# Optimization experiments

Measured on AMD Instinct MI355X. Metric: run time of the kernel, lower is better.

Reference implementation:

```python
import jax, jax.numpy as jnp
import numpy as np

DROPOUT_P = 0.5
HALF_D_LOG_2PI = 8.0  # 0.5 * D * log(2*pi) constant from source, D=16


def _dropout(key, x, p):
    keep = 1.0 - p
    mask = jax.random.bernoulli(key, keep, x.shape).astype(x.dtype)
    return x * mask / keep


def _spmm(adj_vals, row, col, support, n):
    # out[i] = sum_{e: row[e]==i} adj_vals[e] * support[col[e]]
    return jax.ops.segment_sum(adj_vals[:, None] * support[col], row, num_segments=n)


def setup_inputs() -> dict:
    key = jax.random.key(0)
    ks = jax.random.split(key, 9)
    N, F_IN, D, C, E, K = 100000, 512, 16, 16, 3200000, 16
    return {
        "x": jax.random.normal(ks[0], (N, F_IN), dtype=jnp.float32),
        "W1": jax.random.normal(ks[1], (F_IN, D), dtype=jnp.float32) * 0.05,
        "W2": jax.random.normal(ks[2], (D, C), dtype=jnp.float32) * 0.2,
        "adj_vals": jax.random.uniform(ks[3], (E,), dtype=jnp.float32),
        "PI": jax.random.uniform(ks[4], (K,), dtype=jnp.float32, minval=0.01, maxval=1.0),
        "MUs": jax.random.normal(ks[5], (K, D), dtype=jnp.float32),
        "PREs": jax.random.uniform(ks[6], (K, D), dtype=jnp.float32, minval=0.1, maxval=1.0),
        "row": jnp.sort(jax.random.randint(ks[7], (E,), 0, N, dtype=jnp.int32)),
        "col": jax.random.randint(ks[8], (E,), 0, N, dtype=jnp.int32),
    }


def reference(x, W1, W2, adj_vals, PI, MUs, PREs, row, col):
    n = x.shape[0]
    dk1, dk2 = jax.random.split(jax.random.key(42))
    # layer 1: dropout -> linear (P1) -> spmm (P2)
    h = _spmm(adj_vals, row, col, _dropout(dk1, x, DROPOUT_P) @ W1, n)  # [N, D]
    # GMM log-likelihood: log N(h | MU_k, diag(1/PRE_k)) + log PI_k
    diff = h[:, None, :] - MUs[None, :, :]                      # [N, K, D]
    logcomp = (-0.5 * jnp.sum(diff * diff * PREs[None], axis=2)
               + jnp.log(PI)[None, :]
               + 0.5 * jnp.sum(jnp.log(PREs), axis=1)[None, :]
               - HALF_D_LOG_2PI * jnp.log(2.0 * jnp.pi))        # [N, K]
    probs = -jnp.mean(jnp.max(logcomp, axis=1))
    # layer 2: relu -> dropout -> linear -> spmm -> log_softmax
    x1 = jax.nn.relu(h)
    h2 = _spmm(adj_vals, row, col, _dropout(dk2, x1, DROPOUT_P) @ W2, n)  # [N, C]
    return jax.nn.log_softmax(h2, axis=1), probs
```

## Files before the change

### kernel.cpp

```cpp
#include <hip/hip_runtime.h>
#include <stdint.h>

typedef __attribute__((ext_vector_type(8))) short bf16x8;
typedef __attribute__((ext_vector_type(4))) float f32x4;
typedef __attribute__((ext_vector_type(4))) int i32x4;

__host__ __device__ __forceinline__ uint32_t rotl32(uint32_t x, int d){
  return (x << d) | (x >> (32 - d));
}

__host__ __device__ __forceinline__ void threefry2x32(uint32_t k0, uint32_t k1,
                                                      uint32_t x0, uint32_t x1,
                                                      uint32_t* o0, uint32_t* o1){
  uint32_t ks2 = k0 ^ k1 ^ 0x1BD11BDAu;
  x0 += k0; x1 += k1;
  x0 += x1; x1 = rotl32(x1,13); x1 ^= x0;
  x0 += x1; x1 = rotl32(x1,15); x1 ^= x0;
  x0 += x1; x1 = rotl32(x1,26); x1 ^= x0;
  x0 += x1; x1 = rotl32(x1, 6); x1 ^= x0;
  x0 += k1; x1 += ks2 + 1u;
  x0 += x1; x1 = rotl32(x1,17); x1 ^= x0;
  x0 += x1; x1 = rotl32(x1,29); x1 ^= x0;
  x0 += x1; x1 = rotl32(x1,16); x1 ^= x0;
  x0 += x1; x1 = rotl32(x1,24); x1 ^= x0;
  x0 += ks2; x1 += k0 + 2u;
  x0 += x1; x1 = rotl32(x1,13); x1 ^= x0;
  x0 += x1; x1 = rotl32(x1,15); x1 ^= x0;
  x0 += x1; x1 = rotl32(x1,26); x1 ^= x0;
  x0 += x1; x1 = rotl32(x1, 6); x1 ^= x0;
  x0 += k0; x1 += k1 + 3u;
  x0 += x1; x1 = rotl32(x1,17); x1 ^= x0;
  x0 += x1; x1 = rotl32(x1,29); x1 ^= x0;
  x0 += x1; x1 = rotl32(x1,16); x1 ^= x0;
  x0 += x1; x1 = rotl32(x1,24); x1 ^= x0;
  x0 += k1; x1 += ks2 + 4u;
  x0 += x1; x1 = rotl32(x1,13); x1 ^= x0;
  x0 += x1; x1 = rotl32(x1,15); x1 ^= x0;
  x0 += x1; x1 = rotl32(x1,26); x1 ^= x0;
  x0 += x1; x1 = rotl32(x1, 6); x1 ^= x0;
  x0 += ks2; x1 += k0 + 5u;
  *o0 = x0; *o1 = x1;
}

__device__ __forceinline__ uint32_t tf_dropbit(uint32_t k0, uint32_t k1, uint32_t j){
  uint32_t o0, o1;
  threefry2x32(k0, k1, 0u, j, &o0, &o1);
  return (o0 ^ o1) >> 31;
}

__device__ __forceinline__ uint32_t rotl1(uint32_t x, int d){
  return __builtin_amdgcn_alignbit(x, x, (uint32_t)(32 - d));
}

__device__ __forceinline__ ushort f2bf(float f){
  uint32_t u = __float_as_uint(f);
  u += 0x7FFFu + ((u >> 16) & 1u);
  return (ushort)(u >> 16);
}
__device__ __forceinline__ float bf2f(ushort b){
  return __uint_as_float(((uint32_t)b) << 16);
}

__device__ __forceinline__ uint2 drop4(uint32_t k0, uint32_t k1, uint32_t j,
                                       float f0, float f1, float f2, float f3){
  uint32_t ks2 = k0 ^ k1 ^ 0x1BD11BDAu;
  uint32_t xa0 = k0, xa1 = (j + 0u) + k1;
  uint32_t xb0 = k0, xb1 = (j + 1u) + k1;
  uint32_t xc0 = k0, xc1 = (j + 2u) + k1;
  uint32_t xd0 = k0, xd1 = (j + 3u) + k1;
#define RR(d)                                              \
  xa0 += xa1; xa1 = rotl1(xa1, d); xa1 ^= xa0;             \
  xb0 += xb1; xb1 = rotl1(xb1, d); xb1 ^= xb0;             \
  xc0 += xc1; xc1 = rotl1(xc1, d); xc1 ^= xc0;             \
  xd0 += xd1; xd1 = rotl1(xd1, d); xd1 ^= xd0;
#define INJ(ka, kb)                                        \
  { uint32_t A = (ka), B = (kb);                           \
    xa0 += A; xa1 += B; xb0 += A; xb1 += B;                \
    xc0 += A; xc1 += B; xd0 += A; xd1 += B; }
  RR(13) RR(15) RR(26) RR(6)  INJ(k1, ks2 + 1u)
  RR(17) RR(29) RR(16) RR(24) INJ(ks2, k0 + 2u)
  RR(13) RR(15) RR(26) RR(6)  INJ(k0, k1 + 3u)
  RR(17) RR(29) RR(16) RR(24) INJ(k1, ks2 + 4u)
  RR(13) RR(15) RR(26) RR(6)  INJ(ks2, k0 + 5u)
#undef RR
#undef INJ
  uint32_t ba = xa0 ^ xa1, bb = xb0 ^ xb1, bc = xc0 ^ xc1, bd = xd0 ^ xd1;
  uint32_t ua = __float_as_uint(f0) + 0x8000u;
  uint32_t ub = __float_as_uint(f1) + 0x8000u;
  uint32_t uc = __float_as_uint(f2) + 0x8000u;
  uint32_t ud = __float_as_uint(f3) + 0x8000u;
  uint32_t sa = (uint32_t)((int32_t)ba >> 31);
  uint32_t sb = (uint32_t)((int32_t)bb >> 31);
  uint32_t sc = (uint32_t)((int32_t)bc >> 31);
  uint32_t sd = (uint32_t)((int32_t)bd >> 31);
  uint32_t v01 = __builtin_amdgcn_perm(ub, ua, 0x07060302u);
  uint32_t v23 = __builtin_amdgcn_perm(ud, uc, 0x07060302u);
  uint32_t m01 = __builtin_amdgcn_perm(sb, sa, 0x07060302u);
  uint32_t m23 = __builtin_amdgcn_perm(sd, sc, 0x07060302u);
  return make_uint2(v01 & ~m01, v23 & ~m23);
}

__global__ void k_prep(const float* __restrict__ W1, ushort* __restrict__ w1p,
                       const float* __restrict__ PI, const float* __restrict__ PREs,
                       float* __restrict__ ckg){
  int t = threadIdx.x;
  for (int u = 0; u < 32; ++u){
    int idx = u * 256 + t;
    int k = idx >> 4, c = idx & 15;
    w1p[((k >> 3) * 16 + c) * 8 + (k & 7)] = f2bf(2.0f * W1[idx]);
  }
  if (t < 16){
    float s = logf(PI[t]);
    #pragma unroll
    for (int j = 0; j < 16; ++j) s += 0.5f * logf(PREs[t * 16 + j]);
    ckg[t] = s - 8.0f * logf(6.28318530717958647692f);
  }
}

__global__ __launch_bounds__(256, 4) void k_main(
    const float* __restrict__ x, const ushort* __restrict__ w1p,
    ushort* __restrict__ s1, const int* __restrict__ rowv, int* __restrict__ rp,
    uint32_t dk0, uint32_t dk1, int N, int E, int nbG, int nbR){
  __shared__ float part[4][16][17];
  int bid = blockIdx.x;
  if (bid % 5 != 0){
    int rb = bid - bid / 5 - 1;
    if (rb < nbR){
      int e = rb * 256 + threadIdx.x;
      if (e <= E){
        int r0 = (e > 0) ? rowv[e - 1] : -1;
        int r1 = (e < E) ? rowv[e] : N;
        for (int r = r0 + 1; r <= r1; ++r) rp[r] = e;
      }
    }
    return;
  }
  int gb = bid / 5;
  if (gb >= nbG) return;

  int t = threadIdx.x;
  int l = t & 63, w = t >> 6;
  int rA = l & 15, kg = l >> 4;
  int tb = w >> 1, p = w & 1;
  int r0 = gb * 32 + tb * 16;
  int rr = r0 + rA; if (rr > N - 1) rr = N - 1;
  const float4* xv = reinterpret_cast<const float4*>(
      x + (size_t)rr * 512 + (p * 256 + kg * 8));
  uint32_t jb = (uint32_t)rr * 512u + (uint32_t)(p * 256 + kg * 8);

  const bf16x8* bp = reinterpret_cast<const bf16x8*>(w1p);
  bf16x8 Bf[8];
  #pragma unroll
  for (int q = 0; q < 8; ++q) Bf[q] = bp[((p * 8 + q) * 4 + kg) * 16 + rA];

  float4 xa = xv[0], xb = xv[1];
  __builtin_amdgcn_sched_barrier(0);

  f32x4 acc = {0.f, 0.f, 0.f, 0.f};
  #pragma unroll
  for (int ks = 0; ks < 8; ++ks){
    float4 na, nb;
    if (ks < 7){ na = xv[(ks + 1) * 8]; nb = xv[(ks + 1) * 8 + 1]; }
    __builtin_amdgcn_sched_barrier(0);
    uint32_t j0 = jb + (uint32_t)(ks * 32);
    uint2 lo = drop4(dk0, dk1, j0,      xa.x, xa.y, xa.z, xa.w);
    uint2 hi = drop4(dk0, dk1, j0 + 4u, xb.x, xb.y, xb.z, xb.w);
    i32x4 ai = {(int)lo.x, (int)lo.y, (int)hi.x, (int)hi.y};
    bf16x8 a = __builtin_bit_cast(bf16x8, ai);
    acc = __builtin_amdgcn_mfma_f32_16x16x32_bf16(a, Bf[ks], acc, 0, 0, 0);
    if (ks < 7){ xa = na; xb = nb; }
  }

  #pragma unroll
  for (int i2 = 0; i2 < 4; ++i2) part[w][kg * 4 + i2][rA] = acc[i2];
  __syncthreads();
  #pragma unroll
  for (int q = 0; q < 2; ++q){
    int idx = q * 256 + t;
    int tt = idx >> 8, row = (idx >> 4) & 15, col = idx & 15;
    int n = gb * 32 + tt * 16 + row;
    float sum = part[tt * 2][row][col] + part[tt * 2 + 1][row][col];
    if (n < N) s1[(size_t)n * 16 + col] = f2bf(sum);
  }
}

__device__ __forceinline__ float edge_sum(const float* __restrict__ adj,
                                          const int* __restrict__ colv,
                                          const ushort* __restrict__ tbl_d,
                                          int e0, int e1){
  float hs = 0.f;
  int e = e0;
  int ea = (e0 + 3) & ~3; if (ea > e1) ea = e1;
  for (; e < ea; ++e) hs += adj[e] * bf2f(tbl_d[(size_t)colv[e] * 16]);
  float a0 = 0.f, a1 = 0.f, a2 = 0.f, a3 = 0.f;
  float b0 = 0.f, b1 = 0.f, b2 = 0.f, b3 = 0.f;
  for (; e + 8 <= e1; e += 8){
    float4 av = *reinterpret_cast<const float4*>(adj + e);
    int4   cv = *reinterpret_cast<const int4*>(colv + e);
    float4 aw = *reinterpret_cast<const float4*>(adj + e + 4);
    int4   cw = *reinterpret_cast<const int4*>(colv + e + 4);
    a0 += av.x * bf2f(tbl_d[(size_t)cv.x * 16]);
    a1 += av.y * bf2f(tbl_d[(size_t)cv.y * 16]);
    a2 += av.z * bf2f(tbl_d[(size_t)cv.z * 16]);
    a3 += av.w * bf2f(tbl_d[(size_t)cv.w * 16]);
    b0 += aw.x * bf2f(tbl_d[(size_t)cw.x * 16]);
    b1 += aw.y * bf2f(tbl_d[(size_t)cw.y * 16]);
    b2 += aw.z * bf2f(tbl_d[(size_t)cw.z * 16]);
    b3 += aw.w * bf2f(tbl_d[(size_t)cw.w * 16]);
  }
  if (e + 4 <= e1){
    float4 av = *reinterpret_cast<const float4*>(adj + e);
    int4   cv = *reinterpret_cast<const int4*>(colv + e);
    a0 += av.x * bf2f(tbl_d[(size_t)cv.x * 16]);
    a1 += av.y * bf2f(tbl_d[(size_t)cv.y * 16]);
    a2 += av.z * bf2f(tbl_d[(size_t)cv.z * 16]);
    a3 += av.w * bf2f(tbl_d[(size_t)cv.w * 16]);
    e += 4;
  }
  for (; e < e1; ++e) hs += adj[e] * bf2f(tbl_d[(size_t)colv[e] * 16]);
  return hs + ((a0 + b0) + (a1 + b1)) + ((a2 + b2) + (a3 + b3));
}

__global__ __launch_bounds__(256) void k_spmm1(
    const float* __restrict__ adj, const int* __restrict__ colv,
    const int* __restrict__ rp, const ushort* __restrict__ s1,
    const float* __restrict__ MUs, const float* __restrict__ PREs,
    const float* __restrict__ W2, const float* __restrict__ ckg,
    ushort* __restrict__ s2, float* __restrict__ partials,
    uint32_t dk0, uint32_t dk1, int N){
  __shared__ float muT[256], preT[256], w2s[256], ck[16];
  __shared__ float bsum;
  int t = threadIdx.x;
  {
    int j = t >> 4, k = t & 15;
    muT[t]  = MUs[k * 16 + j];
    preT[t] = PREs[k * 16 + j];
  }
  w2s[t] = W2[t];
  if (t < 16) ck[t] = ckg[t];
  if (t == 0) bsum = 0.f;
  __syncthreads();

  int i = blockIdx.x * 16 + (t >> 4);
  int d = t & 15;
  int base = t & 48;
  float h = 0.f;
  if (i < N) h = edge_sum(adj, colv, s1 + d, rp[i], rp[i + 1]);

  float lc = ck[d];
  #pragma unroll
  for (int j = 0; j < 16; ++j){
    float hj = __shfl(h, base + j, 64);
    float df = hj - muT[j * 16 + d];
    lc -= 0.5f * df * df * preT[j * 16 + d];
  }
  float m = lc;
  #pragma unroll
  for (int s = 1; s < 16; s <<= 1) m = fmaxf(m, __shfl_xor(m, s, 64));
  float mrow = (d == 0 && i < N) ? m : 0.f;
  mrow += __shfl_xor(mrow, 16, 64);
  mrow += __shfl_xor(mrow, 32, 64);
  if ((t & 63) == 0) atomicAdd(&bsum, mrow);

  float v = fmaxf(h, 0.f);
  float xd2 = (i < N && !tf_dropbit(dk0, dk1, (uint32_t)i * 16u + (uint32_t)d))
              ? 2.0f * v : 0.f;
  float s2v = 0.f;
  #pragma unroll
  for (int j = 0; j < 16; ++j)
    s2v += __shfl(xd2, base + j, 64) * w2s[j * 16 + d];
  if (i < N) s2[(size_t)i * 16 + d] = f2bf(s2v);
  __syncthreads();
  if (t == 0) partials[blockIdx.x] = bsum;
}

__global__ __launch_bounds__(256) void k_spmm2(
    const float* __restrict__ adj, const int* __restrict__ colv,
    const int* __restrict__ rp, const ushort* __restrict__ s2,
    const float* __restrict__ partials, int nparts,
    float* __restrict__ out, int N){
  int t = threadIdx.x;
  int i = blockIdx.x * 16 + (t >> 4);
  int d = t & 15;
  float h = 0.f;
  if (i < N) h = edge_sum(adj, colv, s2 + d, rp[i], rp[i + 1]);
  float m = h;
  #pragma unroll
  for (int s = 1; s < 16; s <<= 1) m = fmaxf(m, __shfl_xor(m, s, 64));
  float ex = expf(h - m);
  float ssum = ex;
  #pragma unroll
  for (int s = 1; s < 16; s <<= 1) ssum += __shfl_xor(ssum, s, 64);
  if (i < N) out[(size_t)i * 16 + d] = (h - m) - logf(ssum);

  if (blockIdx.x == 0){
    __shared__ float wsum[4];
    float s = 0.f;
    for (int q = t; q < nparts; q += 256) s += partials[q];
    #pragma unroll
    for (int sh = 1; sh < 64; sh <<= 1) s += __shfl_xor(s, sh, 64);
    if ((t & 63) == 0) wsum[t >> 6] = s;
    __syncthreads();
    if (t == 0)
      out[(size_t)N * 16] = -(wsum[0] + wsum[1] + wsum[2] + wsum[3]) / (float)N;
  }
}

extern "C" void kernel_launch(void* const* d_in, const int* in_sizes, int n_in,
                              void* d_out, int out_size, void* d_ws, size_t ws_size,
                              hipStream_t stream){
  const float* x    = (const float*)d_in[0];
  const float* W1   = (const float*)d_in[1];
  const float* W2   = (const float*)d_in[2];
  const float* adj  = (const float*)d_in[3];
  const float* PI   = (const float*)d_in[4];
  const float* MUs  = (const float*)d_in[5];
  const float* PREs = (const float*)d_in[6];
  const int*   rowv = (const int*)d_in[7];
  const int*   colv = (const int*)d_in[8];
  const int N = in_sizes[0] / 512;
  const int E = in_sizes[3];
  float* out = (float*)d_out;

  char* ws = (char*)d_ws;
  float* ckg = (float*)ws;
  int*   rp  = (int*)(ws + 256);
  size_t rpBytes = (((size_t)(N + 1) * 4) + 255) & ~(size_t)255;
  ushort* s1 = (ushort*)(ws + 256 + rpBytes);
  size_t s1Bytes = (((size_t)N * 16 * 2) + 255) & ~(size_t)255;
  ushort* s2 = (ushort*)(ws + 256 + rpBytes + s1Bytes);
  size_t s2Bytes = s1Bytes;
  float* partials = (float*)(ws + 256 + rpBytes + s1Bytes + s2Bytes);
  size_t pBytes = ((((size_t)N / 16 + 1) * 4) + 255) & ~(size_t)255;
  ushort* w1p = (ushort*)(ws + 256 + rpBytes + s1Bytes + s2Bytes + pBytes);

  uint32_t d10, d11, d20, d21;
  threefry2x32(0u, 42u, 0u, 0u, &d10, &d11);
  threefry2x32(0u, 42u, 0u, 1u, &d20, &d21);

  k_prep<<<1, 256, 0, stream>>>(W1, w1p, PI, PREs, ckg);

  int nbG = (N + 31) / 32;
  int nbR = (E + 1 + 255) / 256;
  int grid = 5 * nbG + 2;
  {
    int maxrb = (grid - 1) - (grid - 1) / 5 - 1;
    while (maxrb < nbR - 1){ grid += 2; maxrb = (grid - 1) - (grid - 1) / 5 - 1; }
  }
  k_main<<<grid, 256, 0, stream>>>(x, w1p, s1, rowv, rp, d10, d11, N, E, nbG, nbR);

  int nb2 = (N + 15) / 16;
  k_spmm1<<<nb2, 256, 0, stream>>>(adj, colv, rp, s1, MUs, PREs, W2, ckg,
                                   s2, partials, d20, d21, N);
  k_spmm2<<<nb2, 256, 0, stream>>>(adj, colv, rp, s2, partials, nb2, out, N);
}
```

Baseline: 208.9 us.

## Shrink GEMM tiles to 16 rows, split K across waves, use packed bf16 convert

```diff
diff --git a/kernel.cpp b/kernel.cpp
--- a/kernel.cpp
+++ b/kernel.cpp
@@ -60,6 +60,11 @@
 __device__ __forceinline__ float bf2f(ushort b){
   return __uint_as_float(((uint32_t)b) << 16);
 }
+__device__ __forceinline__ uint32_t cvt_pk_bf16(float lo, float hi){
+  uint32_t r;
+  asm("v_cvt_pk_bf16_f32 %0, %1, %2" : "=v"(r) : "v"(lo), "v"(hi));
+  return r;
+}
 
 __device__ __forceinline__ uint2 drop4(uint32_t k0, uint32_t k1, uint32_t j,
                                        float f0, float f1, float f2, float f3){
@@ -85,16 +90,12 @@
 #undef RR
 #undef INJ
   uint32_t ba = xa0 ^ xa1, bb = xb0 ^ xb1, bc = xc0 ^ xc1, bd = xd0 ^ xd1;
-  uint32_t ua = __float_as_uint(f0) + 0x8000u;
-  uint32_t ub = __float_as_uint(f1) + 0x8000u;
-  uint32_t uc = __float_as_uint(f2) + 0x8000u;
-  uint32_t ud = __float_as_uint(f3) + 0x8000u;
   uint32_t sa = (uint32_t)((int32_t)ba >> 31);
   uint32_t sb = (uint32_t)((int32_t)bb >> 31);
   uint32_t sc = (uint32_t)((int32_t)bc >> 31);
   uint32_t sd = (uint32_t)((int32_t)bd >> 31);
-  uint32_t v01 = __builtin_amdgcn_perm(ub, ua, 0x07060302u);
-  uint32_t v23 = __builtin_amdgcn_perm(ud, uc, 0x07060302u);
+  uint32_t v01 = cvt_pk_bf16(f0, f1);
+  uint32_t v23 = cvt_pk_bf16(f2, f3);
   uint32_t m01 = __builtin_amdgcn_perm(sb, sa, 0x07060302u);
   uint32_t m23 = __builtin_amdgcn_perm(sd, sc, 0x07060302u);
   return make_uint2(v01 & ~m01, v23 & ~m23);
@@ -117,14 +118,15 @@
   }
 }
 
-__global__ __launch_bounds__(256, 4) void k_main(
+__global__ __launch_bounds__(256, 8) void k_main(
     const float* __restrict__ x, const ushort* __restrict__ w1p,
     ushort* __restrict__ s1, const int* __restrict__ rowv, int* __restrict__ rp,
     uint32_t dk0, uint32_t dk1, int N, int E, int nbG, int nbR){
   __shared__ float part[4][16][17];
   int bid = blockIdx.x;
-  if (bid % 5 != 0){
-    int rb = bid - bid / 5 - 1;
+  int m3 = bid % 3;
+  if (m3 != 2){
+    int rb = 2 * (bid / 3) + m3;
     if (rb < nbR){
       int e = rb * 256 + threadIdx.x;
       if (e <= E){
@@ -135,32 +137,31 @@
     }
     return;
   }
-  int gb = bid / 5;
+  int gb = bid / 3;
   if (gb >= nbG) return;
 
   int t = threadIdx.x;
-  int l = t & 63, w = t >> 6;
+  int l = t & 63, p = t >> 6;
   int rA = l & 15, kg = l >> 4;
-  int tb = w >> 1, p = w & 1;
-  int r0 = gb * 32 + tb * 16;
+  int r0 = gb * 16;
   int rr = r0 + rA; if (rr > N - 1) rr = N - 1;
   const float4* xv = reinterpret_cast<const float4*>(
-      x + (size_t)rr * 512 + (p * 256 + kg * 8));
-  uint32_t jb = (uint32_t)rr * 512u + (uint32_t)(p * 256 + kg * 8);
+      x + (size_t)rr * 512 + (p * 128 + kg * 8));
+  uint32_t jb = (uint32_t)rr * 512u + (uint32_t)(p * 128 + kg * 8);
 
   const bf16x8* bp = reinterpret_cast<const bf16x8*>(w1p);
-  bf16x8 Bf[8];
-  #pragma unroll
-  for (int q = 0; q < 8; ++q) Bf[q] = bp[((p * 8 + q) * 4 + kg) * 16 + rA];
+  bf16x8 Bf[4];
+  #pragma unroll
+  for (int q = 0; q < 4; ++q) Bf[q] = bp[((p * 4 + q) * 4 + kg) * 16 + rA];
 
   float4 xa = xv[0], xb = xv[1];
   __builtin_amdgcn_sched_barrier(0);
 
   f32x4 acc = {0.f, 0.f, 0.f, 0.f};
   #pragma unroll
-  for (int ks = 0; ks < 8; ++ks){
+  for (int ks = 0; ks < 4; ++ks){
     float4 na, nb;
-    if (ks < 7){ na = xv[(ks + 1) * 8]; nb = xv[(ks + 1) * 8 + 1]; }
+    if (ks < 3){ na = xv[(ks + 1) * 8]; nb = xv[(ks + 1) * 8 + 1]; }
     __builtin_amdgcn_sched_barrier(0);
     uint32_t j0 = jb + (uint32_t)(ks * 32);
     uint2 lo = drop4(dk0, dk1, j0,      xa.x, xa.y, xa.z, xa.w);
@@ -168,18 +169,17 @@
     i32x4 ai = {(int)lo.x, (int)lo.y, (int)hi.x, (int)hi.y};
     bf16x8 a = __builtin_bit_cast(bf16x8, ai);
     acc = __builtin_amdgcn_mfma_f32_16x16x32_bf16(a, Bf[ks], acc, 0, 0, 0);
-    if (ks < 7){ xa = na; xb = nb; }
-  }
-
-  #pragma unroll
-  for (int i2 = 0; i2 < 4; ++i2) part[w][kg * 4 + i2][rA] = acc[i2];
+    if (ks < 3){ xa = na; xb = nb; }
+  }
+
+  #pragma unroll
+  for (int i2 = 0; i2 < 4; ++i2) part[p][kg * 4 + i2][rA] = acc[i2];
   __syncthreads();
-  #pragma unroll
-  for (int q = 0; q < 2; ++q){
-    int idx = q * 256 + t;
-    int tt = idx >> 8, row = (idx >> 4) & 15, col = idx & 15;
-    int n = gb * 32 + tt * 16 + row;
-    float sum = part[tt * 2][row][col] + part[tt * 2 + 1][row][col];
+  {
+    int row = t >> 4, col = t & 15;
+    int n = r0 + row;
+    float sum = (part[0][row][col] + part[1][row][col])
+              + (part[2][row][col] + part[3][row][col]);
     if (n < N) s1[(size_t)n * 16 + col] = f2bf(sum);
   }
 }
@@ -340,13 +340,11 @@
 
   k_prep<<<1, 256, 0, stream>>>(W1, w1p, PI, PREs, ckg);
 
-  int nbG = (N + 31) / 32;
+  int nbG = N / 16;
   int nbR = (E + 1 + 255) / 256;
-  int grid = 5 * nbG + 2;
-  {
-    int maxrb = (grid - 1) - (grid - 1) / 5 - 1;
-    while (maxrb < nbR - 1){ grid += 2; maxrb = (grid - 1) - (grid - 1) / 5 - 1; }
-  }
+  int grid = 3 * nbG;
+  while (2 * ((grid - 1) / 3) + ((grid - 1) % 3 == 2 ? 0 : (grid - 1) % 3) < nbR - 1)
+    ++grid;
   k_main<<<grid, 256, 0, stream>>>(x, w1p, s1, rowv, rp, d10, d11, N, E, nbG, nbR);
 
   int nb2 = (N + 15) / 16;
```

Measured after the change: 196.1 us (median of 2 runs). -6.2%, faster.
